# Kernel optimization log

Measured on AMD Instinct MI355X. Metric: run time of the kernel, lower is better.

## Reference

```python
import jax, jax.numpy as jnp
import numpy as np

B, L, DH = 4, 4096, 1024
T, DG = 1024, 768
P = 256


def setup_inputs() -> dict:
    key = jax.random.key(0)
    k1, k2, k3, k4, k5 = jax.random.split(key, 5)
    H = jax.random.normal(k1, (B, L, DH), dtype=jnp.float32)
    G = jax.random.normal(k2, (B, T, DG), dtype=jnp.float32)
    # key mask: True = padded/masked. Guarantee at least one valid key per row.
    mask = jax.random.randint(k3, (B, L), 0, 2).astype(jnp.bool_)
    mask = mask.at[:, 0].set(False)
    # torch Linear weights: [out, in]
    Wk_w = jax.random.normal(k4, (P, DH), dtype=jnp.float32) * (DH ** -0.5)
    Wq_w = jax.random.normal(k5, (P, DG), dtype=jnp.float32) * (DG ** -0.5)
    return {"H": H, "G": G, "mask": mask, "Wk_w": Wk_w, "Wq_w": Wq_w}


def reference(H, G, mask, Wk_w, Wq_w):
    # K = Wk(H): [B,L,P]; Q = Wq(G): [B,T,P]
    K = jnp.einsum('bld,pd->blp', H, Wk_w)
    Q = jnp.einsum('btd,pd->btp', G, Wq_w)
    scale = P ** -0.5
    logits = jnp.einsum('btp,blp->btl', Q, K) * scale  # [B,T,L]
    neg_inf = jnp.finfo(logits.dtype).min
    logits = jnp.where(mask[:, None, :], neg_inf, logits)
    alpha = jax.nn.softmax(logits, axis=-1)  # softmax over L (streaming-equivalent)
    Z = jnp.einsum('btl,bld->btd', alpha, H)  # [B,T,DH]
    return Z
```

## Files before the change

### kernel.cpp

```cpp
#include <hip/hip_runtime.h>
#include <hip/hip_bf16.h>


typedef __attribute__((ext_vector_type(8))) short short8;
typedef __attribute__((ext_vector_type(4))) float f32x4;

static __device__ __forceinline__ unsigned short bf16bits(float x) {
    __hip_bfloat16 b = __float2bfloat16(x);
    return *(unsigned short*)&b;
}

static __device__ __forceinline__ void gload_lds16(const __hip_bfloat16* g,
                                                   __hip_bfloat16* l)
{
    auto gp = (const __attribute__((address_space(1))) unsigned int*)(uintptr_t)g;
    auto lp = (__attribute__((address_space(3))) unsigned int*)(unsigned int)(uintptr_t)l;
    __builtin_amdgcn_global_load_lds(gp, lp, 16, 0, 0);
}

__global__ __launch_bounds__(256)
void cvt_f32_bf16_kernel(const float* __restrict__ in,
                         unsigned short* __restrict__ out, int n4)
{
    const int i = blockIdx.x * 256 + threadIdx.x;
    if (i >= n4) return;
    float4 v = ((const float4*)in)[i];
    ushort4 o;
    o.x = bf16bits(v.x); o.y = bf16bits(v.y);
    o.z = bf16bits(v.z); o.w = bf16bits(v.w);
    ((ushort4*)out)[i] = o;
}

__global__ __launch_bounds__(256)
void mask_width_kernel(const unsigned char* __restrict__ m, int* __restrict__ widthOut)
{
    __shared__ int c1, c2, c4, c8, cp;
    if (threadIdx.x == 0) { c1 = c2 = c4 = c8 = cp = 0; }
    __syncthreads();
    int l1 = 0, l2 = 0, l4 = 0, l8 = 0, lp = 0;
    const unsigned short* m16 = (const unsigned short*)m;
    const unsigned int*   m32 = (const unsigned int*)m;
    for (int i = threadIdx.x; i < 16384; i += 256) l1 += (m[i] != 0);
    for (int i = threadIdx.x; i < 8192;  i += 256) {
        l2 += (m16[i] != 0);
        lp += ((m[2 * i] != 0) == (m[2 * i + 1] != 0));
    }
    for (int i = threadIdx.x; i < 4096;  i += 256) l4 += (m32[i] != 0);
    for (int i = threadIdx.x; i < 2048;  i += 256) l8 += ((m32[2 * i] | m32[2 * i + 1]) != 0);
    atomicAdd(&c1, l1); atomicAdd(&c2, l2); atomicAdd(&c4, l4);
    atomicAdd(&c8, l8); atomicAdd(&cp, lp);
    __syncthreads();
    if (threadIdx.x == 0) {
        const float f1 = fabsf(c1 / 16384.f - 0.5f);
        const float f2 = fabsf(c2 / 8192.f  - 0.5f);
        const float f4 = fabsf(c4 / 4096.f  - 0.5f);
        const float f8 = fabsf(c8 / 2048.f  - 0.5f);
        int w = 1; float best = f1;
        if (f2 < best) { best = f2; w = 2; }
        if (f4 < best) { best = f4; w = 4; }
        if (f8 < best) { best = f8; w = 8; }
        if (w == 1 && cp > 7400) w = 2;
        *widthOut = w;
    }
}

__global__ __launch_bounds__(256)
void mask_scan_kernel(const void* __restrict__ mask, const int* __restrict__ widthPtr,
                      unsigned short* __restrict__ idx,
                      int* __restrict__ lc, int* __restrict__ lcpad, int L)
{
    const int b = blockIdx.x;
    const int tid = threadIdx.x;
    const int w = *widthPtr;
    const unsigned char*  m8  = (const unsigned char*)mask;
    const unsigned short* m16 = (const unsigned short*)mask;
    const unsigned int*   m32 = (const unsigned int*)mask;
    const uint2*          m64 = (const uint2*)mask;

    bool v[16];
    int cnt = 0;
    #pragma unroll
    for (int i = 0; i < 16; ++i) {
        const int l = tid * 16 + i;
        const long mi = (long)b * L + l;
        bool masked;
        if (w == 1)      masked = m8[mi] != 0;
        else if (w == 2) masked = m16[mi] != 0;
        else if (w == 4) masked = m32[mi] != 0;
        else             { uint2 q = m64[mi]; masked = (q.x | q.y) != 0; }
        v[i] = !masked;
        cnt += v[i] ? 1 : 0;
    }
    __shared__ int waveTot[4];
    int pre = cnt;
    #pragma unroll
    for (int off = 1; off < 64; off <<= 1) {
        const int t = __shfl_up(pre, off, 64);
        if ((tid & 63) >= off) pre += t;
    }
    if ((tid & 63) == 63) waveTot[tid >> 6] = pre;
    __syncthreads();
    int waveOff = 0;
    for (int wv = 0; wv < (tid >> 6); ++wv) waveOff += waveTot[wv];
    int o = waveOff + pre - cnt;
    #pragma unroll
    for (int i = 0; i < 16; ++i)
        if (v[i]) idx[(long)b * L + (o++)] = (unsigned short)(tid * 16 + i);
    if (tid == 255) {
        const int total = waveOff + pre;
        lc[b] = total;
        lcpad[b] = (total + 127) & ~127;
    }
}

__global__ __launch_bounds__(256)
void h_prep_kernel(const float* __restrict__ H,
                   __hip_bfloat16* __restrict__ Hbf,
                   __hip_bfloat16* __restrict__ Ht,
                   const unsigned short* __restrict__ idx,
                   const int* __restrict__ lc, const int* __restrict__ lcpad,
                   int L, int D)
{
    const int b = blockIdx.z;
    const int c0 = blockIdx.x * 64;
    if (c0 >= lcpad[b]) return;
    const int Lcb = lc[b];
    const float* Hb = H + (long)b * L * D;
    __hip_bfloat16* Hbfb = Hbf + (long)b * L * D;
    __hip_bfloat16* Htb  = Ht  + (long)b * D * L;
    __shared__ __align__(16) __hip_bfloat16 tile[64][72];
    const int d0 = blockIdx.y * 64;
    const int tx = threadIdx.x & 15, ty = threadIdx.x >> 4;
    #pragma unroll
    for (int p = 0; p < 4; ++p) {
        const int row = ty + p * 16;
        const int c = c0 + row;
        float4 v = {0.f, 0.f, 0.f, 0.f};
        if (c < Lcb) {
            const int l = idx[(long)b * L + c];
            v = *(const float4*)(&Hb[(long)l * D + d0 + tx * 4]);
        }
        ushort4 o;
        o.x = bf16bits(v.x); o.y = bf16bits(v.y);
        o.z = bf16bits(v.z); o.w = bf16bits(v.w);
        *(ushort4*)(&Hbfb[(long)c * D + d0 + tx * 4]) = o;
        tile[tx * 4 + 0][row] = __float2bfloat16(v.x);
        tile[tx * 4 + 1][row] = __float2bfloat16(v.y);
        tile[tx * 4 + 2][row] = __float2bfloat16(v.z);
        tile[tx * 4 + 3][row] = __float2bfloat16(v.w);
    }
    __syncthreads();
    const int ll = threadIdx.x & 7;
    const int dq = threadIdx.x >> 3;
    #pragma unroll
    for (int q = 0; q < 2; ++q) {
        const int dd = dq + q * 32;
        const short8 v = *(const short8*)(&tile[dd][ll * 8]);
        *(short8*)(&Htb[(long)(d0 + dd) * L + c0 + ll * 8]) = v;
    }
}

template <typename OutT, int SPLITK, int MODE, int CMODE>
__global__ __launch_bounds__(256)
void gemm_bt_kernel(const __hip_bfloat16* __restrict__ A,
                    const __hip_bfloat16* __restrict__ Bm,
                    OutT* __restrict__ C,
                    int K, int lda, int ldb, int ldc,
                    long batchStrideA, long batchStrideB, long batchStrideC,
                    float scale,
                    float* __restrict__ rowsum,
                    int rowsumStride,
                    long partStride,
                    const int* __restrict__ lc,
                    const int* __restrict__ lcpad,
                    int Lfull)
{
    int bx = blockIdx.x, by = blockIdx.y, bz = blockIdx.z;
    {
        const int nwg = gridDim.x * gridDim.y * gridDim.z;
        if ((nwg & 7) == 0) {
            int lin = bx + gridDim.x * (by + gridDim.y * bz);
            lin = (lin & 7) * (nwg >> 3) + (lin >> 3);
            bx = lin % gridDim.x;
            const int t = lin / gridDim.x;
            by = t % gridDim.y;
            bz = t / gridDim.y;
        }
    }

    const int zb = bz / SPLITK;
    const int kc = bz % SPLITK;
    const int rowBase = bx * 128;
    const int colBase = by * 128;

    if constexpr (CMODE == 1) {
        const int bb = rowBase / Lfull;
        if (rowBase - bb * Lfull >= lcpad[bb]) return;
    }
    if constexpr (CMODE == 2) {
        if (colBase >= lcpad[zb]) return;
    }

    A  += (long)zb * batchStrideA;
    Bm += (long)zb * batchStrideB;
    C  += (long)zb * batchStrideC + (long)kc * partStride;
    int Kdyn = K;
    if constexpr (CMODE == 3) Kdyn = lcpad[zb];
    const int Kloc  = Kdyn / SPLITK;
    const int kbase = kc * Kloc;
    const int NT    = Kloc / 32;

    const int tid  = threadIdx.x;
    const int lane = tid & 63;
    const int wave = tid >> 6;
    const int wm = (wave & 1) * 64;
    const int wn = (wave >> 1) * 64;

    __shared__ __align__(16) __hip_bfloat16 lds_pool[24576];
    __hip_bfloat16* AsP = lds_pool;
    __hip_bfloat16* BsP = lds_pool + 12288;

    f32x4 acc[4][4];
    #pragma unroll
    for (int i = 0; i < 4; ++i)
        #pragma unroll
        for (int j = 0; j < 4; ++j)
            acc[i][j] = (f32x4){0.f, 0.f, 0.f, 0.f};

    const int srow = lane >> 2;
    const int scol = ((lane & 3) ^ ((lane >> 3) & 3)) * 8;
    const long ar0 = (long)(rowBase + wave * 32 + srow) * lda;
    const long ar1 = ar0 + 16l * lda;
    const long br0 = (long)(colBase + wave * 32 + srow) * ldb;
    const long br1 = br0 + 16l * ldb;

    const int mrow = lane & 15;
    const int koff = (((lane >> 4) ^ ((lane >> 1) & 3)) * 8);

    auto stage = [&](int buf, int t) {
        const int kk = kbase + t * 32 + scol;
        gload_lds16(A  + ar0 + kk, AsP + buf * 4096 + wave * 1024);
        gload_lds16(A  + ar1 + kk, AsP + buf * 4096 + wave * 1024 + 512);
        gload_lds16(Bm + br0 + kk, BsP + buf * 4096 + wave * 1024);
        gload_lds16(Bm + br1 + kk, BsP + buf * 4096 + wave * 1024 + 512);
    };

    stage(0, 0);
    if (NT > 1) stage(1, 1);

    int cur = 0;
    for (int t = 0; t < NT; ++t) {
        if (t + 1 < NT)
            asm volatile("s_waitcnt vmcnt(4)" ::: "memory");
        else
            asm volatile("s_waitcnt vmcnt(0)" ::: "memory");
        __builtin_amdgcn_s_barrier();
        if (t + 2 < NT) {
            const int nxt2 = (cur >= 1) ? cur - 1 : cur + 2;
            stage(nxt2, t + 2);
        }

        short8 af[4], bf[4];
        #pragma unroll
        for (int mi = 0; mi < 4; ++mi)
            af[mi] = *(const short8*)(AsP + cur * 4096 + (wm + mi * 16 + mrow) * 32 + koff);
        #pragma unroll
        for (int ni = 0; ni < 4; ++ni)
            bf[ni] = *(const short8*)(BsP + cur * 4096 + (wn + ni * 16 + mrow) * 32 + koff);

        #pragma unroll
        for (int mi = 0; mi < 4; ++mi)
            #pragma unroll
            for (int ni = 0; ni < 4; ++ni)
                acc[mi][ni] = __builtin_amdgcn_mfma_f32_16x16x32_bf16(
                    af[mi], bf[ni], acc[mi][ni], 0, 0, 0);
        cur = (cur == 2) ? 0 : cur + 1;
    }

    const int crow0 = (lane >> 4) * 4;
    const int ccol  = lane & 15;

    if constexpr (MODE == 2 || sizeof(OutT) == 2) {
        __syncthreads();
        __hip_bfloat16* cst = lds_pool;

        if constexpr (MODE == 2) {
            const int lcv = lc[zb];
            bool mk[4];
            #pragma unroll
            for (int ni = 0; ni < 4; ++ni)
                mk[ni] = (colBase + wn + ni * 16 + ccol) >= lcv;
            #pragma unroll
            for (int mi = 0; mi < 4; ++mi) {
                #pragma unroll
                for (int r = 0; r < 4; ++r) {
                    const int row = wm + mi * 16 + crow0 + r;
                    float rs = 0.f;
                    #pragma unroll
                    for (int ni = 0; ni < 4; ++ni) {
                        const int col = wn + ni * 16 + ccol;
                        const float e = mk[ni] ? 0.f
                                               : __expf(acc[mi][ni][r] * scale);
                        const __hip_bfloat16 pb = __float2bfloat16(e);
                        cst[row * 136 + (((col >> 3) ^ (row >> 3)) << 3) + (col & 7)] = pb;
                        rs += __bfloat162float(pb);
                    }
                    rs += __shfl_xor(rs, 1, 64);
                    rs += __shfl_xor(rs, 2, 64);
                    rs += __shfl_xor(rs, 4, 64);
                    rs += __shfl_xor(rs, 8, 64);
                    if ((lane & 15) == 0)
                        atomicAdd(&rowsum[(long)zb * rowsumStride + rowBase + row], rs);
                }
            }
        } else {
            #pragma unroll
            for (int mi = 0; mi < 4; ++mi) {
                #pragma unroll
                for (int ni = 0; ni < 4; ++ni) {
                    #pragma unroll
                    for (int r = 0; r < 4; ++r) {
                        const int row = wm + mi * 16 + crow0 + r;
                        const int col = wn + ni * 16 + ccol;
                        cst[row * 136 + (((col >> 3) ^ (row >> 3)) << 3) + (col & 7)] =
                            __float2bfloat16(acc[mi][ni][r] * scale);
                    }
                }
            }
        }
        __syncthreads();
        const int g   = tid & 15;
        const int r4  = tid >> 4;
        const int lof = ((g ^ r4) << 3);
        #pragma unroll
        for (int k = 0; k < 8; ++k) {
            const int row = r4 * 8 + k;
            const short8 v = *(const short8*)(cst + row * 136 + lof);
            *(short8*)(&((__hip_bfloat16*)C)[(long)(rowBase + row) * ldc + colBase + g * 8]) = v;
        }
    } else {
        #pragma unroll
        for (int mi = 0; mi < 4; ++mi) {
            #pragma unroll
            for (int ni = 0; ni < 4; ++ni) {
                #pragma unroll
                for (int r = 0; r < 4; ++r) {
                    const int row = rowBase + wm + mi * 16 + crow0 + r;
                    const int col = colBase + wn + ni * 16 + ccol;
                    ((float*)C)[(long)row * ldc + col] = acc[mi][ni][r] * scale;
                }
            }
        }
    }
}

__global__ __launch_bounds__(256)
void combine_kernel(const float* __restrict__ Zp,
                    const float* __restrict__ rowsum,
                    float* __restrict__ Z, long partStride)
{
    const int i = blockIdx.x * 256 + threadIdx.x;
    const float4 a = ((const float4*)Zp)[i];
    const float4 b = ((const float4*)(Zp + partStride))[i];
    const float inv = 1.0f / rowsum[i >> 8];
    float4 o;
    o.x = (a.x + b.x) * inv;
    o.y = (a.y + b.y) * inv;
    o.z = (a.z + b.z) * inv;
    o.w = (a.w + b.w) * inv;
    ((float4*)Z)[i] = o;
}

extern "C" void kernel_launch(void* const* d_in, const int* in_sizes, int n_in,
                              void* d_out, int out_size, void* d_ws, size_t ws_size,
                              hipStream_t stream)
{
    constexpr int B = 4, L = 4096, DH = 1024, T = 1024, DG = 768, P = 256;

    const float* H  = (const float*)d_in[0];
    const float* G  = (const float*)d_in[1];
    const void*  mask = d_in[2];
    const float* Wk = (const float*)d_in[3];
    const float* Wq = (const float*)d_in[4];
    for (int i = 0; i < n_in; ++i) {
        switch (in_sizes[i]) {
            case B * L * DH: H    = (const float*)d_in[i]; break;
            case B * T * DG: G    = (const float*)d_in[i]; break;
            case B * L:      mask = d_in[i];               break;
            case P * DH:     Wk   = (const float*)d_in[i]; break;
            case P * DG:     Wq   = (const float*)d_in[i]; break;
        }
    }
    float* Z = (float*)d_out;

    char* ws = (char*)d_ws;
    __hip_bfloat16* Hbf  = (__hip_bfloat16*)ws;
    float*          Zp   = (float*)ws;
    __hip_bfloat16* Ht   = (__hip_bfloat16*)(ws + (32l << 20));
    __hip_bfloat16* Gbf  = (__hip_bfloat16*)(ws + (64l << 20));
    __hip_bfloat16* Qbf  = (__hip_bfloat16*)(ws + (70l << 20));
    __hip_bfloat16* Kbf  = (__hip_bfloat16*)(ws + (72l << 20));
    __hip_bfloat16* Wkbf = (__hip_bfloat16*)(ws + (80l << 20));
    __hip_bfloat16* Wqbf = (__hip_bfloat16*)(ws + (80l << 20) + (512l << 10));
    float*          rowsum    = (float*)(ws + (80l << 20) + (896l << 10));
    int*            widthFlag = (int*)  (ws + (80l << 20) + (960l << 10));
    int*            lcBuf     = (int*)  (ws + (80l << 20) + (961l << 10));
    int*            lcpadBuf  = (int*)  (ws + (80l << 20) + (961l << 10) + 64);
    unsigned short* idxBuf    = (unsigned short*)(ws + (80l << 20) + (962l << 10));
    __hip_bfloat16* Sb   = (__hip_bfloat16*)(ws + (81l << 20));

    constexpr long ZPART = (long)B * T * DH;

    const dim3 blk(256);

    hipMemsetAsync(rowsum, 0, (size_t)(B * T) * sizeof(float), stream);

    mask_width_kernel<<<dim3(1), blk, 0, stream>>>((const unsigned char*)mask, widthFlag);
    mask_scan_kernel<<<dim3(B), blk, 0, stream>>>(mask, widthFlag, idxBuf, lcBuf, lcpadBuf, L);

    h_prep_kernel<<<dim3(L / 64, DH / 64, B), blk, 0, stream>>>(
        H, Hbf, Ht, idxBuf, lcBuf, lcpadBuf, L, DH);
    cvt_f32_bf16_kernel<<<dim3((P * DH) / 1024), blk, 0, stream>>>(Wk, (unsigned short*)Wkbf, (P * DH) / 4);
    cvt_f32_bf16_kernel<<<dim3((P * DG) / 1024), blk, 0, stream>>>(Wq, (unsigned short*)Wqbf, (P * DG) / 4);
    cvt_f32_bf16_kernel<<<dim3((B * T * DG) / 1024), blk, 0, stream>>>(G, (unsigned short*)Gbf, (B * T * DG) / 4);

    gemm_bt_kernel<__hip_bfloat16, 1, 0, 0><<<dim3((B * T) / 128, P / 128, 1), blk, 0, stream>>>(
        Gbf, Wqbf, Qbf, DG, DG, DG, P, 0, 0, 0, 1.0f,
        nullptr, 0, 0, nullptr, nullptr, 0);
    gemm_bt_kernel<__hip_bfloat16, 1, 0, 1><<<dim3((B * L) / 128, P / 128, 1), blk, 0, stream>>>(
        Hbf, Wkbf, Kbf, DH, DH, DH, P, 0, 0, 0, 1.0f,
        nullptr, 0, 0, nullptr, lcpadBuf, L);
    gemm_bt_kernel<__hip_bfloat16, 1, 2, 2><<<dim3(T / 128, L / 128, B), blk, 0, stream>>>(
        Qbf, Kbf, Sb, P, P, P, L,
        (long)T * P, (long)L * P, (long)T * L, 0.0625f,
        rowsum, T, 0, lcBuf, lcpadBuf, L);
    gemm_bt_kernel<float, 2, 0, 3><<<dim3(T / 128, DH / 128, B * 2), blk, 0, stream>>>(
        Sb, Ht, Zp, L, L, L, DH,
        (long)T * L, (long)DH * L, (long)T * DH, 1.0f,
        nullptr, 0, ZPART, nullptr, lcpadBuf, L);
    combine_kernel<<<dim3((B * T * DH / 4) / 256), blk, 0, stream>>>(
        Zp, rowsum, Z, ZPART);
}
```

Before: 239.8 us.

## Merge preprocessing and projection kernels into fewer launches

Folds the rowsum memset and the mask width detection into the per-batch scan kernel, which now runs its width detection redundantly in each of the four blocks. The H gather/transpose and the three fp32-to-bf16 conversions become a single launch that dispatches on block index, and the Q and K projection GEMMs are fused into one grid. The goal is to cut launch overhead and let small grids share the GPU. The cost is duplicated mask reads, plus longer or less regular kernels that may tail worse.

```diff
diff --git a/kernel.cpp b/kernel.cpp
--- a/kernel.cpp
+++ b/kernel.cpp
@@ -19,38 +19,37 @@
 }
 
 __global__ __launch_bounds__(256)
-void cvt_f32_bf16_kernel(const float* __restrict__ in,
-                         unsigned short* __restrict__ out, int n4)
-{
-    const int i = blockIdx.x * 256 + threadIdx.x;
-    if (i >= n4) return;
-    float4 v = ((const float4*)in)[i];
-    ushort4 o;
-    o.x = bf16bits(v.x); o.y = bf16bits(v.y);
-    o.z = bf16bits(v.z); o.w = bf16bits(v.w);
-    ((ushort4*)out)[i] = o;
-}
-
-__global__ __launch_bounds__(256)
-void mask_width_kernel(const unsigned char* __restrict__ m, int* __restrict__ widthOut)
-{
-    __shared__ int c1, c2, c4, c8, cp;
-    if (threadIdx.x == 0) { c1 = c2 = c4 = c8 = cp = 0; }
+void scan_kernel(const void* __restrict__ mask,
+                 unsigned short* __restrict__ idx,
+                 int* __restrict__ lc, int* __restrict__ lcpad,
+                 float* __restrict__ rowsum, int L, int T, int B)
+{
+    const int b = blockIdx.x;
+    const int tid = threadIdx.x;
+
+    for (int i = tid; i < T; i += 256) rowsum[(long)b * T + i] = 0.f;
+
+    const unsigned char*  m8g  = (const unsigned char*)mask;
+    const unsigned short* m16g = (const unsigned short*)mask;
+    const unsigned int*   m32g = (const unsigned int*)mask;
+    __shared__ int c1, c2, c4, c8, cp, wsh;
+    if (tid == 0) { c1 = c2 = c4 = c8 = cp = 0; }
     __syncthreads();
-    int l1 = 0, l2 = 0, l4 = 0, l8 = 0, lp = 0;
-    const unsigned short* m16 = (const unsigned short*)m;
-    const unsigned int*   m32 = (const unsigned int*)m;
-    for (int i = threadIdx.x; i < 16384; i += 256) l1 += (m[i] != 0);
-    for (int i = threadIdx.x; i < 8192;  i += 256) {
-        l2 += (m16[i] != 0);
-        lp += ((m[2 * i] != 0) == (m[2 * i + 1] != 0));
-    }
-    for (int i = threadIdx.x; i < 4096;  i += 256) l4 += (m32[i] != 0);
-    for (int i = threadIdx.x; i < 2048;  i += 256) l8 += ((m32[2 * i] | m32[2 * i + 1]) != 0);
-    atomicAdd(&c1, l1); atomicAdd(&c2, l2); atomicAdd(&c4, l4);
-    atomicAdd(&c8, l8); atomicAdd(&cp, lp);
+    {
+        const int N = B * L;
+        int l1 = 0, l2 = 0, l4 = 0, l8 = 0, lp = 0;
+        for (int i = tid; i < N; i += 256) l1 += (m8g[i] != 0);
+        for (int i = tid; i < N / 2; i += 256) {
+            l2 += (m16g[i] != 0);
+            lp += ((m8g[2 * i] != 0) == (m8g[2 * i + 1] != 0));
+        }
+        for (int i = tid; i < N / 4; i += 256) l4 += (m32g[i] != 0);
+        for (int i = tid; i < N / 8; i += 256) l8 += ((m32g[2 * i] | m32g[2 * i + 1]) != 0);
+        atomicAdd(&c1, l1); atomicAdd(&c2, l2); atomicAdd(&c4, l4);
+        atomicAdd(&c8, l8); atomicAdd(&cp, lp);
+    }
     __syncthreads();
-    if (threadIdx.x == 0) {
+    if (tid == 0) {
         const float f1 = fabsf(c1 / 16384.f - 0.5f);
         const float f2 = fabsf(c2 / 8192.f  - 0.5f);
         const float f4 = fabsf(c4 / 4096.f  - 0.5f);
@@ -60,23 +59,15 @@
         if (f4 < best) { best = f4; w = 4; }
         if (f8 < best) { best = f8; w = 8; }
         if (w == 1 && cp > 7400) w = 2;
-        *widthOut = w;
-    }
-}
-
-__global__ __launch_bounds__(256)
-void mask_scan_kernel(const void* __restrict__ mask, const int* __restrict__ widthPtr,
-                      unsigned short* __restrict__ idx,
-                      int* __restrict__ lc, int* __restrict__ lcpad, int L)
-{
-    const int b = blockIdx.x;
-    const int tid = threadIdx.x;
-    const int w = *widthPtr;
+        wsh = w;
+    }
+    __syncthreads();
+    const int w = wsh;
+
     const unsigned char*  m8  = (const unsigned char*)mask;
     const unsigned short* m16 = (const unsigned short*)mask;
     const unsigned int*   m32 = (const unsigned int*)mask;
     const uint2*          m64 = (const uint2*)mask;
-
     bool v[16];
     int cnt = 0;
     #pragma unroll
@@ -114,80 +105,85 @@
 }
 
 __global__ __launch_bounds__(256)
-void h_prep_kernel(const float* __restrict__ H,
-                   __hip_bfloat16* __restrict__ Hbf,
-                   __hip_bfloat16* __restrict__ Ht,
-                   const unsigned short* __restrict__ idx,
-                   const int* __restrict__ lc, const int* __restrict__ lcpad,
-                   int L, int D)
-{
-    const int b = blockIdx.z;
-    const int c0 = blockIdx.x * 64;
-    if (c0 >= lcpad[b]) return;
-    const int Lcb = lc[b];
-    const float* Hb = H + (long)b * L * D;
-    __hip_bfloat16* Hbfb = Hbf + (long)b * L * D;
-    __hip_bfloat16* Htb  = Ht  + (long)b * D * L;
+void prep_all_kernel(const float* __restrict__ H,
+                     __hip_bfloat16* __restrict__ Hbf,
+                     __hip_bfloat16* __restrict__ Ht,
+                     const unsigned short* __restrict__ idx,
+                     const int* __restrict__ lc, const int* __restrict__ lcpad,
+                     const float* __restrict__ Wk, unsigned short* __restrict__ Wkbf,
+                     const float* __restrict__ Wq, unsigned short* __restrict__ Wqbf,
+                     const float* __restrict__ G,  unsigned short* __restrict__ Gbf,
+                     int L, int D)
+{
     __shared__ __align__(16) __hip_bfloat16 tile[64][72];
-    const int d0 = blockIdx.y * 64;
-    const int tx = threadIdx.x & 15, ty = threadIdx.x >> 4;
-    #pragma unroll
-    for (int p = 0; p < 4; ++p) {
-        const int row = ty + p * 16;
-        const int c = c0 + row;
-        float4 v = {0.f, 0.f, 0.f, 0.f};
-        if (c < Lcb) {
-            const int l = idx[(long)b * L + c];
-            v = *(const float4*)(&Hb[(long)l * D + d0 + tx * 4]);
-        }
-        ushort4 o;
-        o.x = bf16bits(v.x); o.y = bf16bits(v.y);
-        o.z = bf16bits(v.z); o.w = bf16bits(v.w);
-        *(ushort4*)(&Hbfb[(long)c * D + d0 + tx * 4]) = o;
-        tile[tx * 4 + 0][row] = __float2bfloat16(v.x);
-        tile[tx * 4 + 1][row] = __float2bfloat16(v.y);
-        tile[tx * 4 + 2][row] = __float2bfloat16(v.z);
-        tile[tx * 4 + 3][row] = __float2bfloat16(v.w);
-    }
-    __syncthreads();
-    const int ll = threadIdx.x & 7;
-    const int dq = threadIdx.x >> 3;
-    #pragma unroll
-    for (int q = 0; q < 2; ++q) {
-        const int dd = dq + q * 32;
-        const short8 v = *(const short8*)(&tile[dd][ll * 8]);
-        *(short8*)(&Htb[(long)(d0 + dd) * L + c0 + ll * 8]) = v;
-    }
+    int id = blockIdx.x;
+    if (id < 4096) {
+        const int b  = id >> 10;
+        const int c0 = (id & 63) * 64;
+        if (c0 >= lcpad[b]) return;
+        const int d0 = ((id >> 6) & 15) * 64;
+        const int Lcb = lc[b];
+        const float* Hb = H + (long)b * L * D;
+        __hip_bfloat16* Hbfb = Hbf + (long)b * L * D;
+        __hip_bfloat16* Htb  = Ht  + (long)b * D * L;
+        const int tx = threadIdx.x & 15, ty = threadIdx.x >> 4;
+        #pragma unroll
+        for (int p = 0; p < 4; ++p) {
+            const int row = ty + p * 16;
+            const int c = c0 + row;
+            float4 v = {0.f, 0.f, 0.f, 0.f};
+            if (c < Lcb) {
+                const int l = idx[(long)b * L + c];
+                v = *(const float4*)(&Hb[(long)l * D + d0 + tx * 4]);
+            }
+            ushort4 o;
+            o.x = bf16bits(v.x); o.y = bf16bits(v.y);
+            o.z = bf16bits(v.z); o.w = bf16bits(v.w);
+            *(ushort4*)(&Hbfb[(long)c * D + d0 + tx * 4]) = o;
+            tile[tx * 4 + 0][row] = __float2bfloat16(v.x);
+            tile[tx * 4 + 1][row] = __float2bfloat16(v.y);
+            tile[tx * 4 + 2][row] = __float2bfloat16(v.z);
+            tile[tx * 4 + 3][row] = __float2bfloat16(v.w);
+        }
+        __syncthreads();
+        const int ll = threadIdx.x & 7;
+        const int dq = threadIdx.x >> 3;
+        #pragma unroll
+        for (int q = 0; q < 2; ++q) {
+            const int dd = dq + q * 32;
+            const short8 v = *(const short8*)(&tile[dd][ll * 8]);
+            *(short8*)(&Htb[(long)(d0 + dd) * L + c0 + ll * 8]) = v;
+        }
+        return;
+    }
+    id -= 4096;
+    const float* in; unsigned short* out; int n4;
+    if (id < 256)       { in = Wk; out = Wkbf; n4 = (256 * 1024) / 4; }
+    else if (id < 448)  { id -= 256; in = Wq; out = Wqbf; n4 = (256 * 768) / 4; }
+    else                { id -= 448; in = G;  out = Gbf;  n4 = (4 * 1024 * 768) / 4; }
+    const int i = id * 256 + threadIdx.x;
+    if (i >= n4) return;
+    float4 v = ((const float4*)in)[i];
+    ushort4 o;
+    o.x = bf16bits(v.x); o.y = bf16bits(v.y);
+    o.z = bf16bits(v.z); o.w = bf16bits(v.w);
+    ((ushort4*)out)[i] = o;
 }
 
 template <typename OutT, int SPLITK, int MODE, int CMODE>
-__global__ __launch_bounds__(256)
-void gemm_bt_kernel(const __hip_bfloat16* __restrict__ A,
-                    const __hip_bfloat16* __restrict__ Bm,
-                    OutT* __restrict__ C,
-                    int K, int lda, int ldb, int ldc,
-                    long batchStrideA, long batchStrideB, long batchStrideC,
-                    float scale,
-                    float* __restrict__ rowsum,
-                    int rowsumStride,
-                    long partStride,
-                    const int* __restrict__ lc,
-                    const int* __restrict__ lcpad,
-                    int Lfull)
-{
-    int bx = blockIdx.x, by = blockIdx.y, bz = blockIdx.z;
-    {
-        const int nwg = gridDim.x * gridDim.y * gridDim.z;
-        if ((nwg & 7) == 0) {
-            int lin = bx + gridDim.x * (by + gridDim.y * bz);
-            lin = (lin & 7) * (nwg >> 3) + (lin >> 3);
-            bx = lin % gridDim.x;
-            const int t = lin / gridDim.x;
-            by = t % gridDim.y;
-            bz = t / gridDim.y;
-        }
-    }
-
+static __device__ __forceinline__
+void gemm_bt_body(int bx, int by, int bz, __hip_bfloat16* lds_pool,
+                  const __hip_bfloat16* __restrict__ A,
+                  const __hip_bfloat16* __restrict__ Bm,
+                  OutT* __restrict__ C,
+                  int K, int lda, int ldb, int ldc,
+                  long batchStrideA, long batchStrideB, long batchStrideC,
+                  float scale,
+                  float* __restrict__ rowsum, int rowsumStride,
+                  long partStride,
+                  const int* __restrict__ lc, const int* __restrict__ lcpad,
+                  int Lfull)
+{
     const int zb = bz / SPLITK;
     const int kc = bz % SPLITK;
     const int rowBase = bx * 128;
@@ -216,7 +212,6 @@
     const int wm = (wave & 1) * 64;
     const int wn = (wave >> 1) * 64;
 
-    __shared__ __align__(16) __hip_bfloat16 lds_pool[24576];
     __hip_bfloat16* AsP = lds_pool;
     __hip_bfloat16* BsP = lds_pool + 12288;
 
@@ -354,6 +349,65 @@
     }
 }
 
+static __device__ __forceinline__ void xcd_swizzle(int& bx, int& by, int& bz)
+{
+    const int nwg = gridDim.x * gridDim.y * gridDim.z;
+    bx = blockIdx.x; by = blockIdx.y; bz = blockIdx.z;
+    if ((nwg & 7) == 0) {
+        int lin = bx + gridDim.x * (by + gridDim.y * bz);
+        lin = (lin & 7) * (nwg >> 3) + (lin >> 3);
+        bx = lin % gridDim.x;
+        const int t = lin / gridDim.x;
+        by = t % gridDim.y;
+        bz = t / gridDim.y;
+    }
+}
+
+template <typename OutT, int SPLITK, int MODE, int CMODE>
+__global__ __launch_bounds__(256)
+void gemm_bt_kernel(const __hip_bfloat16* __restrict__ A,
+                    const __hip_bfloat16* __restrict__ Bm,
+                    OutT* __restrict__ C,
+                    int K, int lda, int ldb, int ldc,
+                    long batchStrideA, long batchStrideB, long batchStrideC,
+                    float scale,
+                    float* __restrict__ rowsum, int rowsumStride,
+                    long partStride,
+                    const int* __restrict__ lc, const int* __restrict__ lcpad,
+                    int Lfull)
+{
+    __shared__ __align__(16) __hip_bfloat16 lds_pool[24576];
+    int bx, by, bz;
+    xcd_swizzle(bx, by, bz);
+    gemm_bt_body<OutT, SPLITK, MODE, CMODE>(bx, by, bz, lds_pool,
+        A, Bm, C, K, lda, ldb, ldc, batchStrideA, batchStrideB, batchStrideC,
+        scale, rowsum, rowsumStride, partStride, lc, lcpad, Lfull);
+}
+
+__global__ __launch_bounds__(256)
+void qk_gemm_kernel(const __hip_bfloat16* __restrict__ Gbf,
+                    const __hip_bfloat16* __restrict__ Wqbf,
+                    __hip_bfloat16* __restrict__ Qbf,
+                    const __hip_bfloat16* __restrict__ Hbf,
+                    const __hip_bfloat16* __restrict__ Wkbf,
+                    __hip_bfloat16* __restrict__ Kbf,
+                    const int* __restrict__ lcpad,
+                    int DG_, int DH_, int P_, int L_)
+{
+    __shared__ __align__(16) __hip_bfloat16 lds_pool[24576];
+    int bx, by, bz;
+    xcd_swizzle(bx, by, bz);
+    if (bx < 32) {
+        gemm_bt_body<__hip_bfloat16, 1, 0, 0>(bx, by, 0, lds_pool,
+            Gbf, Wqbf, Qbf, DG_, DG_, DG_, P_, 0, 0, 0, 1.0f,
+            nullptr, 0, 0, nullptr, nullptr, 0);
+    } else {
+        gemm_bt_body<__hip_bfloat16, 1, 0, 1>(bx - 32, by, 0, lds_pool,
+            Hbf, Wkbf, Kbf, DH_, DH_, DH_, P_, 0, 0, 0, 1.0f,
+            nullptr, 0, 0, nullptr, lcpad, L_);
+    }
+}
+
 __global__ __launch_bounds__(256)
 void combine_kernel(const float* __restrict__ Zp,
                     const float* __restrict__ rowsum,
@@ -403,7 +457,6 @@
     __hip_bfloat16* Wkbf = (__hip_bfloat16*)(ws + (80l << 20));
     __hip_bfloat16* Wqbf = (__hip_bfloat16*)(ws + (80l << 20) + (512l << 10));
     float*          rowsum    = (float*)(ws + (80l << 20) + (896l << 10));
-    int*            widthFlag = (int*)  (ws + (80l << 20) + (960l << 10));
     int*            lcBuf     = (int*)  (ws + (80l << 20) + (961l << 10));
     int*            lcpadBuf  = (int*)  (ws + (80l << 20) + (961l << 10) + 64);
     unsigned short* idxBuf    = (unsigned short*)(ws + (80l << 20) + (962l << 10));
@@ -413,23 +466,17 @@
 
     const dim3 blk(256);
 
-    hipMemsetAsync(rowsum, 0, (size_t)(B * T) * sizeof(float), stream);
-
-    mask_width_kernel<<<dim3(1), blk, 0, stream>>>((const unsigned char*)mask, widthFlag);
-    mask_scan_kernel<<<dim3(B), blk, 0, stream>>>(mask, widthFlag, idxBuf, lcBuf, lcpadBuf, L);
-
-    h_prep_kernel<<<dim3(L / 64, DH / 64, B), blk, 0, stream>>>(
-        H, Hbf, Ht, idxBuf, lcBuf, lcpadBuf, L, DH);
-    cvt_f32_bf16_kernel<<<dim3((P * DH) / 1024), blk, 0, stream>>>(Wk, (unsigned short*)Wkbf, (P * DH) / 4);
-    cvt_f32_bf16_kernel<<<dim3((P * DG) / 1024), blk, 0, stream>>>(Wq, (unsigned short*)Wqbf, (P * DG) / 4);
-    cvt_f32_bf16_kernel<<<dim3((B * T * DG) / 1024), blk, 0, stream>>>(G, (unsigned short*)Gbf, (B * T * DG) / 4);
-
-    gemm_bt_kernel<__hip_bfloat16, 1, 0, 0><<<dim3((B * T) / 128, P / 128, 1), blk, 0, stream>>>(
-        Gbf, Wqbf, Qbf, DG, DG, DG, P, 0, 0, 0, 1.0f,
-        nullptr, 0, 0, nullptr, nullptr, 0);
-    gemm_bt_kernel<__hip_bfloat16, 1, 0, 1><<<dim3((B * L) / 128, P / 128, 1), blk, 0, stream>>>(
-        Hbf, Wkbf, Kbf, DH, DH, DH, P, 0, 0, 0, 1.0f,
-        nullptr, 0, 0, nullptr, lcpadBuf, L);
+    scan_kernel<<<dim3(B), blk, 0, stream>>>(
+        mask, idxBuf, lcBuf, lcpadBuf, rowsum, L, T, B);
+
+    prep_all_kernel<<<dim3(7616), blk, 0, stream>>>(
+        H, Hbf, Ht, idxBuf, lcBuf, lcpadBuf,
+        Wk, (unsigned short*)Wkbf, Wq, (unsigned short*)Wqbf,
+        G, (unsigned short*)Gbf, L, DH);
+
+    qk_gemm_kernel<<<dim3(160, 2, 1), blk, 0, stream>>>(
+        Gbf, Wqbf, Qbf, Hbf, Wkbf, Kbf, lcpadBuf, DG, DH, P, L);
+
     gemm_bt_kernel<__hip_bfloat16, 1, 2, 2><<<dim3(T / 128, L / 128, B), blk, 0, stream>>>(
         Qbf, Kbf, Sb, P, P, P, L,
         (long)T * P, (long)L * P, (long)T * L, 0.0625f,
```

Result: faster. 219.9 us (-8.3%).
